# Performance work log

Measured on AMD Instinct MI355X. Metric: run time of the kernel, lower is better.

The kernel has to match this reference:

```python
import jax, jax.numpy as jnp
import numpy as np

B, T, D = 2, 2048, 2048
HK, HV, K, V = 16, 32, 128, 128          # key heads, value heads, head dims
KEY_DIM, VALUE_DIM = HK * K, HV * V      # 2048, 4096
CONV_W = 4                               # causal conv kernel width
EPS = 1e-6


def setup_inputs() -> dict:
    key = jax.random.key(0)
    ks = jax.random.split(key, 8)
    rn = lambda k, shp, sc: jax.random.normal(k, shp, dtype=jnp.float32) * sc
    return {
        "hidden_states": rn(ks[0], (B, T, D), 1.0),
        "W_qkvz": rn(ks[1], (D, 2 * KEY_DIM + 2 * VALUE_DIM), D ** -0.5),
        "W_ba": rn(ks[2], (D, 2 * HV), D ** -0.5),
        "conv_weight": rn(ks[3], (2 * KEY_DIM + VALUE_DIM, CONV_W), CONV_W ** -0.5),
        "A_log": jnp.log(jax.random.uniform(ks[4], (HV,), minval=1.0, maxval=16.0)),
        "dt_bias": rn(ks[5], (HV,), 0.5),
        "norm_weight": jnp.zeros((V,), jnp.float32),  # zero-centered RMSNorm weight
        "W_out": rn(ks[6], (VALUE_DIM, D), VALUE_DIM ** -0.5),
    }


def _l2norm(x):
    return x * jax.lax.rsqrt(jnp.sum(x * x, axis=-1, keepdims=True) + 1e-6)


def _causal_conv_silu(x, w):
    # x: [B,T,C]; depthwise causal conv, kernel width CONV_W, then SiLU
    xp = jnp.pad(x, ((0, 0), (CONV_W - 1, 0), (0, 0)))
    out = sum(xp[:, j:j + x.shape[1], :] * w[None, None, :, j] for j in range(CONV_W))
    return jax.nn.silu(out)


def _gated_delta_rule(q, k, v, g, beta):
    # q,k: [B,T,HV,K] (l2-normed, q pre-scaled); v: [B,T,HV,V]; g,beta: [B,T,HV]
    def step(S, xs):                      # S: [B,HV,K,V]
        q_t, k_t, v_t, g_t, beta_t = xs
        S = S * jnp.exp(g_t)[..., None, None]
        pred = jnp.einsum('bhk,bhkv->bhv', k_t, S)
        delta = (v_t - pred) * beta_t[..., None]
        S = S + jnp.einsum('bhk,bhv->bhkv', k_t, delta)
        o_t = jnp.einsum('bhk,bhkv->bhv', q_t, S)
        return S, o_t

    mv = lambda x: jnp.moveaxis(x, 1, 0)  # time-major for scan
    S0 = jnp.zeros((q.shape[0], HV, K, V), q.dtype)
    _, o = jax.lax.scan(step, S0, (mv(q), mv(k), mv(v), mv(g), mv(beta)))
    return jnp.moveaxis(o, 0, 1)          # [B,T,HV,V]


def reference(hidden_states, W_qkvz, W_ba, conv_weight, A_log, dt_bias,
              norm_weight, W_out):
    b_, t_ = hidden_states.shape[:2]
    qkvz = hidden_states @ W_qkvz
    q, k, v, z = jnp.split(qkvz, [KEY_DIM, 2 * KEY_DIM, 2 * KEY_DIM + VALUE_DIM], axis=-1)
    ba = hidden_states @ W_ba
    b_gate, a = jnp.split(ba, 2, axis=-1)  # each [B,T,HV]

    # fused causal conv1d + SiLU over concat(q,k,v)
    mixed = _causal_conv_silu(jnp.concatenate([q, k, v], axis=-1), conv_weight)
    q, k, v = jnp.split(mixed, [KEY_DIM, 2 * KEY_DIM], axis=-1)

    # gating: beta = sigmoid(b), g = -exp(A_log) * softplus(a + dt_bias)
    beta = jax.nn.sigmoid(b_gate)
    g = -jnp.exp(A_log) * jax.nn.softplus(a + dt_bias)

    # GQA expand (v_per_k_group = HV // HK), l2norm, scale
    rep = HV // HK
    q = jnp.repeat(q.reshape(b_, t_, HK, K), rep, axis=2)
    k = jnp.repeat(k.reshape(b_, t_, HK, K), rep, axis=2)
    v = v.reshape(b_, t_, HV, V)
    q = _l2norm(q) * (K ** -0.5)
    k = _l2norm(k)

    o = _gated_delta_rule(q, k, v, g, beta)  # [B,T,HV,V]

    # gated RMSNorm (per value head, zero-centered weight) then out projection
    zg = z.reshape(b_, t_, HV, V)
    x = o * jax.nn.silu(zg)
    var = jnp.mean(x * x, axis=-1, keepdims=True)
    x = x * jax.lax.rsqrt(var + EPS) * (1.0 + norm_weight)
    return x.reshape(b_, t_, VALUE_DIM) @ W_out
```

## Files before the change

kernel.cpp:

```cpp
#include <hip/hip_runtime.h>

typedef unsigned short u16;
typedef unsigned int u32;

typedef short bf16x8 __attribute__((ext_vector_type(8)));
typedef float f32x4 __attribute__((ext_vector_type(4)));
typedef float f32x16 __attribute__((ext_vector_type(16)));

#define T_SEQ 2048
#define MFMA16(a, b, c) __builtin_amdgcn_mfma_f32_16x16x32_bf16(a, b, c, 0, 0, 0)
#define MFMA32(a, b, c) __builtin_amdgcn_mfma_f32_32x32x16_bf16(a, b, c, 0, 0, 0)

__device__ __forceinline__ u16 f2bf(float f) {
    u32 u = __float_as_uint(f);
    u += 0x7fffu + ((u >> 16) & 1u);
    return (u16)(u >> 16);
}
__device__ __forceinline__ float bf2f(u16 s) {
    return __uint_as_float(((u32)s) << 16);
}
__device__ __forceinline__ void g2lds16(const u16* gp, u16* lp) {
    __builtin_amdgcn_global_load_lds((const __attribute__((address_space(1))) void*)gp,
                                     (__attribute__((address_space(3))) void*)lp, 16, 0, 0);
}

__global__ __launch_bounds__(256) void cast_f32_bf16(const float* __restrict__ in,
                                                     u16* __restrict__ out, long n) {
    long i = ((long)blockIdx.x * 256 + threadIdx.x) * 4;
    if (i + 3 < n) {
        float4 v = *(const float4*)&in[i];
        out[i + 0] = f2bf(v.x);
        out[i + 1] = f2bf(v.y);
        out[i + 2] = f2bf(v.z);
        out[i + 3] = f2bf(v.w);
    }
}

__global__ __launch_bounds__(256) void transpose_cast(const float* __restrict__ in,
                                                      u16* __restrict__ out, int R, int C) {
    __shared__ float tile[32][33];
    int c0 = blockIdx.x * 32, r0 = blockIdx.y * 32;
    int tx = threadIdx.x & 31, ty = threadIdx.x >> 5;
#pragma unroll
    for (int rr = 0; rr < 32; rr += 8)
        tile[ty + rr][tx] = in[(long)(r0 + ty + rr) * C + c0 + tx];
    __syncthreads();
#pragma unroll
    for (int rr = 0; rr < 32; rr += 8)
        out[(long)(c0 + ty + rr) * R + r0 + tx] = f2bf(tile[tx][ty + rr]);
}

template <int MODE>
__global__ __launch_bounds__(256) void gemm_bt(const u16* __restrict__ A,
                                               const u16* __restrict__ B, void* __restrict__ C,
                                               void* __restrict__ C2, int M, int N, int K, int lda,
                                               int ldb, int ldc) {
    __shared__ __align__(16) u16 As[128 * 64];
    __shared__ __align__(16) u16 Bs[128 * 64];
    int m0 = blockIdx.x * 128, n0 = blockIdx.y * 128;
    int tid = threadIdx.x;
    int lane = tid & 63, w = tid >> 6;
    int wr = w >> 1, wc = w & 1;
    int l31 = lane & 31, hf = lane >> 5;

    f32x16 acc[2][2];
#pragma unroll
    for (int mi = 0; mi < 2; mi++)
#pragma unroll
        for (int nj = 0; nj < 2; nj++)
#pragma unroll
            for (int r = 0; r < 16; r++) acc[mi][nj][r] = 0.f;

    int srow = tid >> 3;
    int sc8 = ((tid & 7) ^ ((tid >> 3) & 7)) * 8;
    const u16* Ag = &A[(long)(m0 + srow) * lda + sc8];
    const u16* Bg = &B[(long)(n0 + srow) * ldb + sc8];

    for (int k0 = 0; k0 < K; k0 += 64) {
#pragma unroll
        for (int p = 0; p < 4; p++) {
            g2lds16(Ag + (long)p * 32 * lda + k0, &As[(p * 256 + tid) * 8]);
            g2lds16(Bg + (long)p * 32 * ldb + k0, &Bs[(p * 256 + tid) * 8]);
        }
        __syncthreads();
#pragma unroll
        for (int ks = 0; ks < 4; ks++) {
            int cell = ((ks * 2 + hf) ^ (l31 & 7)) * 8;
            bf16x8 a0 = *(const bf16x8*)&As[(wr * 64 + l31) * 64 + cell];
            bf16x8 a1 = *(const bf16x8*)&As[(wr * 64 + 32 + l31) * 64 + cell];
            bf16x8 b0 = *(const bf16x8*)&Bs[(wc * 64 + l31) * 64 + cell];
            bf16x8 b1 = *(const bf16x8*)&Bs[(wc * 64 + 32 + l31) * 64 + cell];
            acc[0][0] = MFMA32(a0, b0, acc[0][0]);
            acc[0][1] = MFMA32(a0, b1, acc[0][1]);
            acc[1][0] = MFMA32(a1, b0, acc[1][0]);
            acc[1][1] = MFMA32(a1, b1, acc[1][1]);
        }
        __syncthreads();
    }

    if (MODE == 0) {
#pragma unroll
        for (int mi = 0; mi < 2; mi++)
#pragma unroll
            for (int nj = 0; nj < 2; nj++)
#pragma unroll
                for (int r = 0; r < 16; r++) {
                    int row = m0 + wr * 64 + mi * 32 + (r >> 2) * 8 + hf * 4 + (r & 3);
                    int col = n0 + wc * 64 + nj * 32 + l31;
                    ((float*)C)[(long)row * ldc + col] = acc[mi][nj][r];
                }
    } else {
        u16* dst;
        long dldc;
        int ncol0;
        if (MODE == 2 && n0 >= 8192) {
            dst = (u16*)C2;
            dldc = 4096;
            ncol0 = n0 - 8192;
        } else {
            dst = (u16*)C;
            dldc = (MODE == 2) ? 8192 : ldc;
            ncol0 = n0;
        }
#pragma unroll 1
        for (int half_e = 0; half_e < 2; half_e++) {
            __syncthreads();
            if (wc == half_e) {
#pragma unroll
                for (int mi = 0; mi < 2; mi++)
#pragma unroll
                    for (int nj = 0; nj < 2; nj++)
#pragma unroll
                        for (int r = 0; r < 16; r++) {
                            int row = wr * 64 + mi * 32 + (r >> 2) * 8 + hf * 4 + (r & 3);
                            int col = nj * 32 + l31;
                            u16* base = (row < 64) ? As : Bs;
                            base[(row & 63) * 64 + col] = f2bf(acc[mi][nj][r]);
                        }
            }
            __syncthreads();
#pragma unroll
            for (int rr = 0; rr < 4; rr++) {
                int row = rr * 32 + (tid >> 3), seg = tid & 7;
                u16* base = (row < 64) ? As : Bs;
                *(uint4*)&dst[(long)(m0 + row) * dldc + ncol0 + half_e * 64 + seg * 8] =
                    *(uint4*)&base[(row & 63) * 64 + seg * 8];
            }
        }
    }
}

__global__ __launch_bounds__(256) void ba_gemm(const u16* __restrict__ hid,
                                               const u16* __restrict__ WbaT,
                                               const float* __restrict__ A_log,
                                               const float* __restrict__ dt_bias,
                                               float* __restrict__ g, float* __restrict__ beta) {
    __shared__ __align__(16) u16 As2[32 * 40];
    __shared__ __align__(16) u16 Bs2[64 * 40];
    int m0 = blockIdx.x * 32;
    int tid = threadIdx.x, lane = tid & 63, w = tid >> 6;
    int quad = lane >> 4, l15 = lane & 15;
    int trow = w & 1;
    int ctile = (w >> 1) * 2;
    f32x4 acc[2];
    acc[0] = (f32x4){0.f, 0.f, 0.f, 0.f};
    acc[1] = (f32x4){0.f, 0.f, 0.f, 0.f};
    int srow = tid >> 2, sc8 = (tid & 3) * 8;
    for (int k0 = 0; k0 < 2048; k0 += 32) {
        if (tid < 128)
            *(uint4*)&As2[srow * 40 + sc8] =
                *(const uint4*)&hid[(long)(m0 + srow) * 2048 + k0 + sc8];
        *(uint4*)&Bs2[srow * 40 + sc8] = *(const uint4*)&WbaT[(long)srow * 2048 + k0 + sc8];
        __syncthreads();
        bf16x8 a = *(const bf16x8*)&As2[(trow * 16 + l15) * 40 + quad * 8];
#pragma unroll
        for (int j = 0; j < 2; j++) {
            bf16x8 b = *(const bf16x8*)&Bs2[((ctile + j) * 16 + l15) * 40 + quad * 8];
            acc[j] = MFMA16(a, b, acc[j]);
        }
        __syncthreads();
    }
#pragma unroll
    for (int j = 0; j < 2; j++)
#pragma unroll
        for (int r = 0; r < 4; r++) {
            int tok = m0 + trow * 16 + quad * 4 + r;
            int col = (ctile + j) * 16 + l15;
            float tot = acc[j][r];
            if (col < 32) {
                beta[(long)tok * 32 + col] = 1.f / (1.f + expf(-tot));
            } else {
                int h = col - 32;
                float x = tot + dt_bias[h];
                float sp = (x > 20.f) ? x : log1pf(expf(x));
                g[(long)tok * 32 + h] = -expf(A_log[h]) * sp;
            }
        }
}

__global__ __launch_bounds__(256) void conv_gate(const u16* __restrict__ qkv,
                                                 const float* __restrict__ conv_w,
                                                 u16* __restrict__ qn, u16* __restrict__ kn,
                                                 u16* __restrict__ vc) {
    int tok = blockIdx.x, tid = threadIdx.x;
    int tloc = tok & (T_SEQ - 1);
    __shared__ float mixed[8192];
    __shared__ float sh_norm[32];
    uint4 zero4;
    zero4.x = zero4.y = zero4.z = zero4.w = 0u;
#pragma unroll
    for (int i = 0; i < 4; i++) {
        int c = (i * 256 + tid) * 8;
        long base = (long)tok * 8192 + c;
        uint4 x3 = *(const uint4*)&qkv[base];
        uint4 x2 = (tloc >= 1) ? *(const uint4*)&qkv[base - 8192] : zero4;
        uint4 x1 = (tloc >= 2) ? *(const uint4*)&qkv[base - 16384] : zero4;
        uint4 x0 = (tloc >= 3) ? *(const uint4*)&qkv[base - 24576] : zero4;
        const u16* p0 = (const u16*)&x0;
        const u16* p1 = (const u16*)&x1;
        const u16* p2 = (const u16*)&x2;
        const u16* p3 = (const u16*)&x3;
#pragma unroll
        for (int e = 0; e < 8; e++) {
            float4 wv = *(const float4*)&conv_w[(long)(c + e) * 4];
            float a = bf2f(p0[e]) * wv.x + bf2f(p1[e]) * wv.y + bf2f(p2[e]) * wv.z +
                      bf2f(p3[e]) * wv.w;
            mixed[c + e] = a / (1.f + __expf(-a));
        }
    }
    __syncthreads();
    int grp = tid >> 3, sub = tid & 7;
    float ss = 0.f;
#pragma unroll
    for (int e = 0; e < 16; e++) {
        float v = mixed[grp * 128 + sub * 16 + e];
        ss += v * v;
    }
    ss += __shfl_xor(ss, 4, 8);
    ss += __shfl_xor(ss, 2, 8);
    ss += __shfl_xor(ss, 1, 8);
    if (sub == 0) sh_norm[grp] = rsqrtf(ss + 1e-6f);
    __syncthreads();
#pragma unroll
    for (int i = 0; i < 4; i++) {
        int c = (i * 256 + tid) * 8;
        float nf = (c < 2048) ? sh_norm[c >> 7] * 0.08838834764831845f
                              : ((c < 4096) ? sh_norm[c >> 7] : 1.f);
        u16 ob[8];
#pragma unroll
        for (int e = 0; e < 8; e++) ob[e] = f2bf(mixed[c + e] * nf);
        uint4 val = *(uint4*)ob;
        if (c < 2048)
            *(uint4*)&qn[(long)tok * 2048 + c] = val;
        else if (c < 4096)
            *(uint4*)&kn[(long)tok * 2048 + (c - 2048)] = val;
        else
            *(uint4*)&vc[(long)tok * 4096 + (c - 4096)] = val;
    }
}

__global__ __launch_bounds__(256) void phaseA(const u16* __restrict__ qn,
                                              const u16* __restrict__ kn,
                                              const u16* __restrict__ vc,
                                              const float* __restrict__ g,
                                              const float* __restrict__ beta,
                                              u16* __restrict__ Tv_g, u16* __restrict__ Tw_g,
                                              u16* __restrict__ Q2_g, u16* __restrict__ obuf) {
    __shared__ __align__(16) u16 kbuf[64][136];
    __shared__ __align__(16) float BMt[64][68];
    __shared__ __align__(16) u16 YT[256][72];
    u16* Lbf = &kbuf[0][0];

    int bid = blockIdx.x;
    int c = bid & 31, h = (bid >> 5) & 31, b = bid >> 10;
    int hk = h >> 1;
    long tokbase = (long)b * T_SEQ + c * 64;
    long cb = (long)bid * 8192;
    int tid = threadIdx.x, lane = tid & 63, w = tid >> 6;
    int quad = lane >> 4, l15 = lane & 15;

    float gl = g[(tokbase + lane) * 32 + h];
    float bl = beta[(tokbase + lane) * 32 + h];
    float cgl = gl;
#pragma unroll
    for (int d = 1; d < 64; d <<= 1) {
        float y = __shfl_up(cgl, d);
        if (lane >= d) cgl += y;
    }
    float wscl = bl * __expf(cgl);
    float eCgl = __expf(cgl);

#pragma unroll
    for (int p = 0; p < 4; p++) {
        int u = p * 256 + tid;
        int row = u >> 4, col8 = (u & 15) * 8;
        *(uint4*)&kbuf[row][col8] = *(const uint4*)&kn[(tokbase + row) * 2048 + hk * 128 + col8];
    }
    __syncthreads();

    {
        f32x4 gk[4];
#pragma unroll
        for (int nj = 0; nj < 4; nj++) gk[nj] = (f32x4){0.f, 0.f, 0.f, 0.f};
#pragma unroll
        for (int kk = 0; kk < 4; kk++) {
            bf16x8 a = *(const bf16x8*)&kbuf[w * 16 + l15][kk * 32 + quad * 8];
#pragma unroll
            for (int nj = 0; nj < 4; nj++) {
                bf16x8 bb = *(const bf16x8*)&kbuf[nj * 16 + l15][kk * 32 + quad * 8];
                gk[nj] = MFMA16(a, bb, gk[nj]);
            }
        }
#pragma unroll
        for (int nj = 0; nj < 4; nj++)
#pragma unroll
            for (int r = 0; r < 4; r++) {
                int i = w * 16 + quad * 4 + r;
                int j = nj * 16 + l15;
                float cgi = __shfl(cgl, i), cgj = __shfl(cgl, j);
                float bi = __shfl(bl, i);
                BMt[j][i] = (j < i) ? bi * gk[nj][r] * __expf(cgi - cgj) : 0.f;
            }
    }
    __syncthreads();

    {
        int col = tid;
        bool isV = col < 128;
        int kcol = col & 127;
        long vbase = tokbase * 4096 + h * 128 + kcol;
        float Yreg[8], acc8[8];
#pragma unroll 1
        for (int bi = 0; bi < 8; ++bi) {
            float vr[8];
            if (isV) {
#pragma unroll
                for (int ii = 0; ii < 8; ii++)
                    vr[ii] = bf2f(vc[vbase + (long)(bi * 8 + ii) * 4096]);
            }
#pragma unroll
            for (int ii = 0; ii < 8; ii++) acc8[ii] = 0.f;
            for (int j = 0; j < bi * 8; ++j) {
                float yv = bf2f(YT[col][j]);
                float4 m0 = *(const float4*)&BMt[j][bi * 8];
                float4 m1 = *(const float4*)&BMt[j][bi * 8 + 4];
                acc8[0] += m0.x * yv;
                acc8[1] += m0.y * yv;
                acc8[2] += m0.z * yv;
                acc8[3] += m0.w * yv;
                acc8[4] += m1.x * yv;
                acc8[5] += m1.y * yv;
                acc8[6] += m1.z * yv;
                acc8[7] += m1.w * yv;
            }
            u16 outb[8];
#pragma unroll
            for (int ii = 0; ii < 8; ii++) {
                int i = bi * 8 + ii;
                float rhs = isV ? __shfl(bl, i) * vr[ii] : __shfl(wscl, i) * bf2f(kbuf[i][kcol]);
                float s = rhs - acc8[ii];
#pragma unroll
                for (int jj = 0; jj < 8; jj++)
                    if (jj < ii) s -= BMt[bi * 8 + jj][i] * Yreg[jj];
                Yreg[ii] = s;
                outb[ii] = f2bf(s);
            }
            *(uint4*)&YT[col][bi * 8] = *(uint4*)outb;
#pragma unroll
            for (int ii = 0; ii < 8; ii++) {
                if (isV)
                    Tv_g[cb + (bi * 8 + ii) * 128 + kcol] = outb[ii];
                else
                    Tw_g[cb + (bi * 8 + ii) * 128 + kcol] = outb[ii];
            }
        }
    }
    __syncthreads();

    {
        f32x4 qk_[4];
#pragma unroll
        for (int nj = 0; nj < 4; nj++) qk_[nj] = (f32x4){0.f, 0.f, 0.f, 0.f};
#pragma unroll
        for (int kk = 0; kk < 4; kk++) {
            bf16x8 a = *(const bf16x8*)&qn[(tokbase + w * 16 + l15) * 2048 + hk * 128 + kk * 32 +
                                           quad * 8];
#pragma unroll
            for (int nj = 0; nj < 4; nj++) {
                bf16x8 bb = *(const bf16x8*)&kbuf[nj * 16 + l15][kk * 32 + quad * 8];
                qk_[nj] = MFMA16(a, bb, qk_[nj]);
            }
        }
        __syncthreads();
#pragma unroll
        for (int nj = 0; nj < 4; nj++)
#pragma unroll
            for (int r = 0; r < 4; r++) {
                int t = w * 16 + quad * 4 + r;
                int rr = nj * 16 + l15;
                float cgt = __shfl(cgl, t), cgr = __shfl(cgl, rr);
                float val = (rr <= t) ? qk_[nj][r] * __expf(cgt - cgr) : 0.f;
                Lbf[t * 72 + rr] = f2bf(val);
            }
    }
    __syncthreads();

#pragma unroll 1
    for (int half = 0; half < 2; half++) {
        f32x4 oa[8];
#pragma unroll
        for (int nj = 0; nj < 8; nj++) oa[nj] = (f32x4){0.f, 0.f, 0.f, 0.f};
#pragma unroll
        for (int kk = 0; kk < 2; kk++) {
            bf16x8 a = *(const bf16x8*)&Lbf[(w * 16 + l15) * 72 + kk * 32 + quad * 8];
#pragma unroll
            for (int nj = 0; nj < 8; nj++) {
                bf16x8 bb = *(const bf16x8*)&YT[half * 128 + nj * 16 + l15][kk * 32 + quad * 8];
                oa[nj] = MFMA16(a, bb, oa[nj]);
            }
        }
        if (half == 0) {
#pragma unroll
            for (int nj = 0; nj < 8; nj++)
#pragma unroll
                for (int r = 0; r < 4; r++) {
                    int t = w * 16 + quad * 4 + r;
                    int vcol = nj * 16 + l15;
                    obuf[(tokbase + t) * 4096 + h * 128 + vcol] = f2bf(oa[nj][r]);
                }
        } else {
#pragma unroll
            for (int nj = 0; nj < 8; nj++)
#pragma unroll
                for (int r = 0; r < 4; r++) {
                    int t = w * 16 + quad * 4 + r;
                    int kcol = nj * 16 + l15;
                    float qsc = __shfl(eCgl, t);
                    float qv = bf2f(qn[(tokbase + t) * 2048 + hk * 128 + kcol]);
                    Q2_g[cb + t * 128 + kcol] = f2bf(qsc * qv - oa[nj][r]);
                }
        }
    }
}

__global__ __launch_bounds__(256) void phaseB(const u16* __restrict__ kn,
                                              const float* __restrict__ g,
                                              const u16* __restrict__ Tv_g,
                                              const u16* __restrict__ Tw_g,
                                              const u16* __restrict__ Q2_g,
                                              u16* __restrict__ obuf) {
    __shared__ __align__(16) float Sf[128][32];
    __shared__ __align__(16) u16 SbfT[32][136];
    __shared__ __align__(16) u16 KhT[128][72];
    __shared__ __align__(16) u16 Ut[32][72];

    int bid = blockIdx.x;
    int vq = bid & 3, h = (bid >> 2) & 31, b = bid >> 7;
    int hk = h >> 1;
    int tid = threadIdx.x, lane = tid & 63, w = tid >> 6;
    int quad = lane >> 4, l15 = lane & 15;

    for (int p = tid; p < 128 * 32; p += 256) ((float*)Sf)[p] = 0.f;
    for (int p = tid; p < 32 * 136; p += 256) ((u16*)SbfT)[p] = 0;
    __syncthreads();

    float gl_pf;
    uint4 kreg[4];
    bf16x8 aTw[4], aQ2[4];
    u16 tvv_pf[2][4], oold[2][4];

#define PB_PREFETCH(cc)                                                                      \
    {                                                                                        \
        long tb_ = (long)b * T_SEQ + (cc) * 64;                                              \
        long cb_ = ((long)((b * 32 + h) * 32) + (cc)) * 8192;                                \
        gl_pf = g[(tb_ + lane) * 32 + h];                                                    \
        const u16* kp_ = &kn[(tb_ + lane) * 2048 + hk * 128 + w * 32];                       \
        kreg[0] = *(const uint4*)&kp_[0];                                                    \
        kreg[1] = *(const uint4*)&kp_[8];                                                    \
        kreg[2] = *(const uint4*)&kp_[16];                                                   \
        kreg[3] = *(const uint4*)&kp_[24];                                                   \
        _Pragma("unroll") for (int kk = 0; kk < 4; kk++) {                                   \
            aTw[kk] = *(const bf16x8*)&Tw_g[cb_ + (w * 16 + l15) * 128 + kk * 32 + quad * 8]; \
            aQ2[kk] = *(const bf16x8*)&Q2_g[cb_ + (w * 16 + l15) * 128 + kk * 32 + quad * 8]; \
        }                                                                                    \
        _Pragma("unroll") for (int nj = 0; nj < 2; nj++) _Pragma("unroll")                   \
            for (int r = 0; r < 4; r++) {                                                    \
            int i_ = w * 16 + quad * 4 + r;                                                  \
            int vg_ = vq * 32 + nj * 16 + l15;                                               \
            tvv_pf[nj][r] = Tv_g[cb_ + (long)i_ * 128 + vg_];                                \
            oold[nj][r] = obuf[(tb_ + i_) * 4096 + h * 128 + vg_];                           \
        }                                                                                    \
    }

    PB_PREFETCH(0);

    for (int c = 0; c < 32; ++c) {
        long tokbase = (long)b * T_SEQ + c * 64;
        float cgl = gl_pf;
#pragma unroll
        for (int d = 1; d < 64; d <<= 1) {
            float y = __shfl_up(cgl, d);
            if (lane >= d) cgl += y;
        }
        float cgC = __shfl(cgl, 63);
        float A_C = __expf(cgC);
        float kscl = __expf(cgC - cgl);

        {
            const u16* kk16 = (const u16*)kreg;
#pragma unroll
            for (int j = 0; j < 32; j++) KhT[w * 32 + j][lane] = f2bf(bf2f(kk16[j]) * kscl);
        }

        f32x4 y1[2], oo[2];
#pragma unroll
        for (int nj = 0; nj < 2; nj++) {
            y1[nj] = (f32x4){0.f, 0.f, 0.f, 0.f};
            oo[nj] = (f32x4){0.f, 0.f, 0.f, 0.f};
        }
#pragma unroll
        for (int kk = 0; kk < 4; kk++) {
#pragma unroll
            for (int nj = 0; nj < 2; nj++) {
                bf16x8 bb = *(const bf16x8*)&SbfT[nj * 16 + l15][kk * 32 + quad * 8];
                y1[nj] = MFMA16(aTw[kk], bb, y1[nj]);
                oo[nj] = MFMA16(aQ2[kk], bb, oo[nj]);
            }
        }
#pragma unroll
        for (int nj = 0; nj < 2; nj++)
#pragma unroll
            for (int r = 0; r < 4; r++) {
                int i = w * 16 + quad * 4 + r;
                int vl = nj * 16 + l15;
                int vg = vq * 32 + vl;
                Ut[vl][i] = f2bf(bf2f(tvv_pf[nj][r]) - y1[nj][r]);
                obuf[(tokbase + i) * 4096 + h * 128 + vg] = f2bf(bf2f(oold[nj][r]) + oo[nj][r]);
            }
        __syncthreads();

        if (c + 1 < 32) PB_PREFETCH(c + 1);

#pragma unroll
        for (int mm = 0; mm < 2; mm++) {
            int mi = 2 * w + mm;
#pragma unroll
            for (int nj = 0; nj < 2; nj++) {
                f32x4 sacc;
#pragma unroll
                for (int r = 0; r < 4; r++)
                    sacc[r] = A_C * Sf[mi * 16 + quad * 4 + r][nj * 16 + l15];
#pragma unroll
                for (int kk = 0; kk < 2; kk++) {
                    bf16x8 a = *(const bf16x8*)&KhT[mi * 16 + l15][kk * 32 + quad * 8];
                    bf16x8 bb = *(const bf16x8*)&Ut[nj * 16 + l15][kk * 32 + quad * 8];
                    sacc = MFMA16(a, bb, sacc);
                }
#pragma unroll
                for (int r = 0; r < 4; r++) {
                    int kd = mi * 16 + quad * 4 + r, vl = nj * 16 + l15;
                    Sf[kd][vl] = sacc[r];
                    SbfT[vl][kd] = f2bf(sacc[r]);
                }
            }
        }
        __syncthreads();
    }
#undef PB_PREFETCH
}

__global__ __launch_bounds__(256) void gated_norm(const u16* __restrict__ obuf,
                                                  const u16* __restrict__ zbuf,
                                                  const float* __restrict__ norm_w,
                                                  u16* __restrict__ xn) {
    int tok = blockIdx.x, tid = threadIdx.x;
    long obase = (long)tok * 4096 + tid * 16;
    u16 ob[16], zb[16];
    *(uint4*)(ob + 0) = *(const uint4*)&obuf[obase];
    *(uint4*)(ob + 8) = *(const uint4*)&obuf[obase + 8];
    *(uint4*)(zb + 0) = *(const uint4*)&zbuf[obase];
    *(uint4*)(zb + 8) = *(const uint4*)&zbuf[obase + 8];
    float x[16];
    float ss = 0.f;
#pragma unroll
    for (int i = 0; i < 16; i++) {
        float ov = bf2f(ob[i]);
        float zv = bf2f(zb[i]);
        float xv = ov * (zv / (1.f + expf(-zv)));
        x[i] = xv;
        ss += xv * xv;
    }
    ss += __shfl_xor(ss, 4, 8);
    ss += __shfl_xor(ss, 2, 8);
    ss += __shfl_xor(ss, 1, 8);
    float scale = rsqrtf(ss * (1.f / 128.f) + 1e-6f);
    int cbase = (tid * 16) & 127;
#pragma unroll
    for (int i = 0; i < 16; i++)
        xn[(long)tok * 4096 + tid * 16 + i] = f2bf(x[i] * scale * (1.f + norm_w[cbase + i]));
}

extern "C" void kernel_launch(void* const* d_in, const int* in_sizes, int n_in, void* d_out,
                              int out_size, void* d_ws, size_t ws_size, hipStream_t stream) {
    const float* hidden = (const float*)d_in[0];
    const float* W_qkvz = (const float*)d_in[1];
    const float* W_ba = (const float*)d_in[2];
    const float* conv_w = (const float*)d_in[3];
    const float* A_log = (const float*)d_in[4];
    const float* dt_bias = (const float*)d_in[5];
    const float* norm_w = (const float*)d_in[6];
    const float* W_out = (const float*)d_in[7];
    float* out = (float*)d_out;

    char* ws = (char*)d_ws;
    u16* wqT = (u16*)(ws + 0);
    u16* qn = (u16*)(ws + 0);
    u16* vc = (u16*)(ws + 16777216L);
    u16* hidbf = (u16*)(ws + 50331648L);
    u16* kn = (u16*)(ws + 50331648L);
    u16* woT = (u16*)(ws + 67108864L);
    u16* qkv_raw = (u16*)(ws + 83886080L);
    u16* Tv = (u16*)(ws + 83886080L);
    u16* Tw = (u16*)(ws + 117440512L);
    u16* xn = (u16*)(ws + 83886080L);
    u16* WbaT = (u16*)(ws + 150994944L);
    u16* zbuf = (u16*)(ws + 150994944L);
    u16* Q2 = (u16*)(ws + 184549376L);
    float* g = (float*)(ws + 218103808L);
    float* beta = (float*)(ws + 218628096L);
    u16* obuf = vc;

    cast_f32_bf16<<<8192, 256, 0, stream>>>(hidden, hidbf, 8388608L);
    transpose_cast<<<dim3(384, 64), 256, 0, stream>>>(W_qkvz, wqT, 2048, 12288);
    transpose_cast<<<dim3(64, 128), 256, 0, stream>>>(W_out, woT, 4096, 2048);
    transpose_cast<<<dim3(2, 64), 256, 0, stream>>>(W_ba, WbaT, 2048, 64);
    ba_gemm<<<128, 256, 0, stream>>>(hidbf, WbaT, A_log, dt_bias, g, beta);
    gemm_bt<2><<<dim3(32, 96), 256, 0, stream>>>(hidbf, wqT, qkv_raw, zbuf, 4096, 12288, 2048,
                                                 2048, 2048, 0);
    conv_gate<<<4096, 256, 0, stream>>>(qkv_raw, conv_w, qn, kn, vc);
    phaseA<<<2048, 256, 0, stream>>>(qn, kn, vc, g, beta, Tv, Tw, Q2, obuf);
    phaseB<<<256, 256, 0, stream>>>(kn, g, Tv, Tw, Q2, obuf);
    gated_norm<<<4096, 256, 0, stream>>>(obuf, zbuf, norm_w, xn);
    gemm_bt<0><<<dim3(32, 16), 256, 0, stream>>>(xn, woT, out, nullptr, 4096, 2048, 4096, 4096,
                                                 4096, 2048);
}
```

Measured before the change: 964.1 us.

## Replace QKVZ projection GEMM with 256x256-tile 4-stage pipelined MFMA kernel

Adds a dedicated gemm256 kernel for the 4096x12288x2048 input projection. It uses 256x256 output tiles, 512 threads, and a 4-deep LDS ring filled by direct global-to-LDS loads with explicit vmcnt waits. It also adds an XOR-swizzled epilogue and a grouped block order for L2 reuse. The larger tiles cut global traffic per FLOP and overlap loads with MFMA, at the cost of 128KB of LDS and heavy register use that limit occupancy, plus hardcoded shapes.

```diff
diff --git a/kernel.cpp b/kernel.cpp
--- a/kernel.cpp
+++ b/kernel.cpp
@@ -147,6 +147,155 @@
                     *(uint4*)&base[(row & 63) * 64 + seg * 8];
             }
         }
+    }
+}
+
+#define VM8 asm volatile("s_waitcnt vmcnt(8)" ::: "memory")
+#define VM4 asm volatile("s_waitcnt vmcnt(4)" ::: "memory")
+#define VM0 asm volatile("s_waitcnt vmcnt(0)" ::: "memory")
+#define VMNONE ((void)0)
+
+#define STAGE_A(S, R2)                       \
+    do {                                     \
+        u16* Ld = &sbuf[(R2) * 16384];       \
+        long ko = (long)(S) * 32;            \
+        g2lds16(pA0 + ko, Ld + dA0);         \
+        g2lds16(pA1 + ko, Ld + dA1);         \
+    } while (0)
+#define STAGE_B(S, R2)                          \
+    do {                                        \
+        u16* Ld = &sbuf[(R2) * 16384 + 8192];   \
+        long ko = (long)(S) * 32;               \
+        g2lds16(pB0 + ko, Ld + dA0);            \
+        g2lds16(pB1 + ko, Ld + dA1);            \
+    } while (0)
+
+#define MQUAD(RB, AV)                          \
+    acc[RB][0] = MFMA16(AV, b0, acc[RB][0]);   \
+    acc[RB][1] = MFMA16(AV, b1, acc[RB][1]);   \
+    acc[RB][2] = MFMA16(AV, b2, acc[RB][2]);   \
+    acc[RB][3] = MFMA16(AV, b3, acc[RB][3]);
+
+#define GITER(RING, S3, STG, VMSTMT)                                        \
+    {                                                                       \
+        const u16* LA = &sbuf[(RING) * 16384 + wm8 * 512 + lane8];          \
+        const u16* LB = &sbuf[(RING) * 16384 + 8192 + wn4 * 512 + lane8];   \
+        bf16x8 b0 = *(const bf16x8*)&LB[0];                                 \
+        bf16x8 b1 = *(const bf16x8*)&LB[512];                               \
+        bf16x8 b2 = *(const bf16x8*)&LB[1024];                              \
+        bf16x8 b3 = *(const bf16x8*)&LB[1536];                              \
+        bf16x8 a0 = *(const bf16x8*)&LA[0];                                 \
+        bf16x8 a1 = *(const bf16x8*)&LA[512];                               \
+        bf16x8 a2 = *(const bf16x8*)&LA[1024];                              \
+        bf16x8 a3 = *(const bf16x8*)&LA[1536];                              \
+        if (STG) STAGE_A(S3, ((RING) + 3) & 3);                             \
+        __builtin_amdgcn_sched_barrier(0);                                  \
+        __builtin_amdgcn_s_barrier();                                       \
+        asm volatile("s_waitcnt lgkmcnt(0)" ::: "memory");                  \
+        __builtin_amdgcn_sched_barrier(0);                                  \
+        __builtin_amdgcn_s_setprio(1);                                      \
+        MQUAD(0, a0)                                                        \
+        MQUAD(1, a1)                                                        \
+        MQUAD(2, a2)                                                        \
+        MQUAD(3, a3)                                                        \
+        __builtin_amdgcn_s_setprio(0);                                      \
+        __builtin_amdgcn_s_barrier();                                       \
+        a0 = *(const bf16x8*)&LA[2048];                                     \
+        a1 = *(const bf16x8*)&LA[2560];                                     \
+        a2 = *(const bf16x8*)&LA[3072];                                     \
+        a3 = *(const bf16x8*)&LA[3584];                                     \
+        if (STG) STAGE_B(S3, ((RING) + 3) & 3);                             \
+        __builtin_amdgcn_sched_barrier(0);                                  \
+        __builtin_amdgcn_s_barrier();                                       \
+        asm volatile("s_waitcnt lgkmcnt(0)" ::: "memory");                  \
+        __builtin_amdgcn_sched_barrier(0);                                  \
+        __builtin_amdgcn_s_setprio(1);                                      \
+        MQUAD(4, a0)                                                        \
+        MQUAD(5, a1)                                                        \
+        MQUAD(6, a2)                                                        \
+        MQUAD(7, a3)                                                        \
+        __builtin_amdgcn_s_setprio(0);                                      \
+        VMSTMT;                                                             \
+        __builtin_amdgcn_s_barrier();                                       \
+    }
+
+__global__ __launch_bounds__(512, 2) void gemm256(const u16* __restrict__ A,
+                                                  const u16* __restrict__ B,
+                                                  u16* __restrict__ Cq, u16* __restrict__ Cz) {
+    __shared__ __align__(16) u16 sbuf[65536];
+    int bid = blockIdx.x;
+    int swz = (bid & 7) * 96 + (bid >> 3);
+    int m0 = (swz & 15) * 256;
+    int n0 = (swz >> 4) * 256;
+    int tid = threadIdx.x;
+    int lane = tid & 63, w = tid >> 6;
+    int l15 = lane & 15, quad = lane >> 4;
+    int wm8 = (w >> 2) * 8, wn4 = (w & 3) * 4;
+    int lane8 = lane * 8;
+    int dA0 = w * 512 + lane8, dA1 = w * 512 + lane8 + 4096;
+    const u16* pA0 = &A[(long)(m0 + w * 16 + l15) * 2048 + quad * 8];
+    const u16* pA1 = pA0 + 128L * 2048;
+    const u16* pB0 = &B[(long)(n0 + w * 16 + l15) * 2048 + quad * 8];
+    const u16* pB1 = pB0 + 128L * 2048;
+
+    f32x4 acc[8][4];
+#pragma unroll
+    for (int i = 0; i < 8; i++)
+#pragma unroll
+        for (int j = 0; j < 4; j++) acc[i][j] = (f32x4){0.f, 0.f, 0.f, 0.f};
+
+    STAGE_A(0, 0);
+    STAGE_B(0, 0);
+    STAGE_A(1, 1);
+    STAGE_B(1, 1);
+    STAGE_A(2, 2);
+    STAGE_B(2, 2);
+    VM8;
+    __builtin_amdgcn_s_barrier();
+
+    for (int it = 0; it < 60; it += 4) {
+        GITER(0, it + 3, 1, VM8);
+        GITER(1, it + 4, 1, VM8);
+        GITER(2, it + 5, 1, VM8);
+        GITER(3, it + 6, 1, VM8);
+    }
+    GITER(0, 63, 1, VM8);
+    GITER(1, 0, 0, VM4);
+    GITER(2, 0, 0, VM0);
+    GITER(3, 0, 0, VMNONE);
+
+#pragma unroll
+    for (int rb = 0; rb < 8; rb++)
+#pragma unroll
+        for (int cb = 0; cb < 4; cb++)
+#pragma unroll
+            for (int r = 0; r < 4; r++) {
+                int row = wm8 * 16 + rb * 16 + quad * 4 + r;
+                int col = wn4 * 16 + cb * 16 + l15;
+                int cg = col >> 4;
+                int phys = row * 256 + ((cg ^ (row & 7)) << 4) + (col & 15);
+                sbuf[phys] = f2bf(acc[rb][cb][r]);
+            }
+    __syncthreads();
+    u16* dst;
+    long dldc;
+    int ncol0;
+    if (n0 >= 8192) {
+        dst = Cz;
+        dldc = 4096;
+        ncol0 = n0 - 8192;
+    } else {
+        dst = Cq;
+        dldc = 8192;
+        ncol0 = n0;
+    }
+#pragma unroll
+    for (int p = 0; p < 16; p++) {
+        int row = p * 16 + (tid >> 5);
+        int seg = tid & 31;
+        int cg = seg >> 1;
+        int phys = row * 256 + ((cg ^ (row & 7)) << 4) + (seg & 1) * 8;
+        *(uint4*)&dst[(long)(m0 + row) * dldc + ncol0 + seg * 8] = *(const uint4*)&sbuf[phys];
     }
 }
 
@@ -635,8 +784,7 @@
     transpose_cast<<<dim3(64, 128), 256, 0, stream>>>(W_out, woT, 4096, 2048);
     transpose_cast<<<dim3(2, 64), 256, 0, stream>>>(W_ba, WbaT, 2048, 64);
     ba_gemm<<<128, 256, 0, stream>>>(hidbf, WbaT, A_log, dt_bias, g, beta);
-    gemm_bt<2><<<dim3(32, 96), 256, 0, stream>>>(hidbf, wqT, qkv_raw, zbuf, 4096, 12288, 2048,
-                                                 2048, 2048, 0);
+    gemm256<<<768, 512, 0, stream>>>(hidbf, wqT, qkv_raw, zbuf);
     conv_gate<<<4096, 256, 0, stream>>>(qkv_raw, conv_w, qn, kn, vc);
     phaseA<<<2048, 256, 0, stream>>>(qn, kn, vc, g, beta, Tv, Tw, Q2, obuf);
     phaseB<<<256, 256, 0, stream>>>(kn, g, Tv, Tw, Q2, obuf);
```

Result: faster. 935.0 us (-3.0%).
